# Optimization experiments

Hardware: AMD Instinct MI355X
Metric: run time of the kernel (lower is better)

The kernel has to match this reference:

```python
import jax, jax.numpy as jnp
import numpy as np


def setup_inputs() -> dict:
    key = jax.random.key(0)
    ks = jax.random.split(key, 6)
    B, H, W, C = 8, 128, 128, 256
    x = jax.random.normal(ks[0], (B, H, W), dtype=jnp.float32)
    atten_x_full = jax.random.normal(ks[1], (B, H, W, W), dtype=jnp.float32)
    atten_y_full = jax.random.normal(ks[2], (B, W, H, H), dtype=jnp.float32)
    value_full = jax.random.normal(ks[3], (B, H, W, C), dtype=jnp.float32)
    # nn.Parameter init: shift = |randn|, bias = -|randn|
    shift = jnp.abs(jax.random.normal(ks[4], (1,), dtype=jnp.float32))
    bias = -jnp.abs(jax.random.normal(ks[5], (1,), dtype=jnp.float32))
    return {"x": x, "atten_x_full": atten_x_full, "atten_y_full": atten_y_full,
            "value_full": value_full, "shift": shift, "bias": bias}


def reference(x, atten_x_full, atten_y_full, value_full, shift, bias):
    H, W = x.shape[1], x.shape[2]
    # Gaussian distance biases: gx[c, h] = -(shift*(h-c)^2 + bias), gy[r, w] likewise
    hw = jnp.arange(W, dtype=jnp.float32)
    hh = jnp.arange(H, dtype=jnp.float32)
    gx = -(shift[0] * (hw[None, :] - hw[:, None]) ** 2 + bias[0])  # [W, W]
    gy = -(shift[0] * (hh[None, :] - hh[:, None]) ** 2 + bias[0])  # [H, H]
    # atten_x_full indexed [b, r, c, k] -> add gx[c, k]; softmax over k (row direction)
    Ax = jax.nn.softmax(atten_x_full + gx[None, None, :, :], axis=-1)  # [B,H,W,W]
    # atten_y_full indexed [b, c, r, k] -> add gy[r, k]; softmax over k (col direction)
    Ay = jax.nn.softmax(atten_y_full + gy[None, None, :, :], axis=-1)  # [B,W,H,H]
    out = (jnp.einsum('brck,brkd->brcd', Ax, value_full)
           + jnp.einsum('bcrk,bkcd->brcd', Ay, value_full))  # [B,H,W,C]
    return out
```

## Files before the change

### kernel.cpp

```cpp
#include <hip/hip_runtime.h>
#include <hip/hip_bf16.h>

typedef __attribute__((ext_vector_type(8))) short short8;
typedef __attribute__((ext_vector_type(4))) float floatx4;
typedef __attribute__((ext_vector_type(2))) float floatx2;

#define LDK 136

__device__ __forceinline__ unsigned short f2bf(float x) {
    unsigned u = __builtin_bit_cast(unsigned, x);
    return (unsigned short)((u + 0x7fffu + ((u >> 16) & 1u)) >> 16);
}

template <bool ACCUM>
__global__ __launch_bounds__(512) void gtrans(
    const float* __restrict__ atten, const float* __restrict__ value,
    float* __restrict__ out, const float* __restrict__ shiftp,
    const float* __restrict__ biasp, int s0, int s1)
{
    __shared__ short Buf[128 * LDK];

    const int bi   = blockIdx.x;
    const int b    = bi >> 7;
    const int i    = bi & 127;
    const int tid  = threadIdx.x;
    const int lane = tid & 63;
    const int w    = tid >> 6;

    const float shift = shiftp[0];
    const float bias  = biasp[0];

    const float* abase = atten + (size_t)bi * (128 * 128);
    const float* vbase = value + (size_t)b * (128 * 128 * 256) + (size_t)i * s0;
    float*       obase = out   + (size_t)b * (128 * 128 * 256) + (size_t)i * s0;

    {
        floatx2 v[16];
#pragma unroll
        for (int j = 0; j < 16; ++j) {
            int c = w * 16 + j;
            v[j] = *(const floatx2*)(abase + c * 128 + 2 * lane);
        }
#pragma unroll
        for (int j = 0; j < 16; ++j) {
            int c = w * 16 + j;
            float d0 = (float)(2 * lane)     - (float)c;
            float d1 = (float)(2 * lane + 1) - (float)c;
            float a0 = v[j].x - (shift * d0 * d0 + bias);
            float a1 = v[j].y - (shift * d1 * d1 + bias);
            float m = fmaxf(a0, a1);
#pragma unroll
            for (int s = 1; s < 64; s <<= 1) m = fmaxf(m, __shfl_xor(m, s, 64));
            float e0 = __expf(a0 - m);
            float e1 = __expf(a1 - m);
            float ssum = e0 + e1;
#pragma unroll
            for (int s = 1; s < 64; s <<= 1) ssum += __shfl_xor(ssum, s, 64);
            float r = 1.0f / ssum;
            unsigned p = (unsigned)f2bf(e0 * r) | ((unsigned)f2bf(e1 * r) << 16);
            *(unsigned*)(&Buf[c * LDK + 2 * lane]) = p;
        }
    }
    __syncthreads();

    short8 bfrag[4];
    {
        int n  = w * 16 + (lane & 15);
        int kq = (lane >> 4) * 8;
#pragma unroll
        for (int ks = 0; ks < 4; ++ks)
            bfrag[ks] = *(const short8*)(&Buf[n * LDK + ks * 32 + kq]);
    }
    __syncthreads();

    floatx4 acc[8];
    const int am = lane & 15;
    const int kq = (lane >> 4) * 8;
#pragma unroll
    for (int half = 0; half < 2; ++half) {
        {
            floatx2 vv[16];
#pragma unroll
            for (int j = 0; j < 16; ++j) {
                int k = w * 16 + j;
                vv[j] = *(const floatx2*)(vbase + (size_t)k * s1 + half * 128 + 2 * lane);
            }
#pragma unroll
            for (int j = 0; j < 16; ++j) {
                int k  = w * 16 + j;
                int dl = 2 * lane;
                Buf[dl * LDK + k]       = (short)f2bf(vv[j].x);
                Buf[(dl + 1) * LDK + k] = (short)f2bf(vv[j].y);
            }
        }
        __syncthreads();

#pragma unroll
        for (int t = 0; t < 8; ++t) acc[t] = (floatx4)0.0f;

#pragma unroll
        for (int ks = 0; ks < 4; ++ks) {
#pragma unroll
            for (int t = 0; t < 8; ++t) {
                short8 af = *(const short8*)(&Buf[(t * 16 + am) * LDK + ks * 32 + kq]);
                acc[t] = __builtin_amdgcn_mfma_f32_16x16x32_bf16(af, bfrag[ks], acc[t], 0, 0, 0);
            }
        }

        {
            int n = w * 16 + (lane & 15);
            float* orow = obase + (size_t)n * s1 + half * 128 + (lane >> 4) * 4;
#pragma unroll
            for (int t = 0; t < 8; ++t) {
                float* p = orow + t * 16;
                floatx4 res = acc[t];
                if (ACCUM) {
                    floatx4 old = *(const floatx4*)p;
                    res = res + old;
                }
                *(floatx4*)p = res;
            }
        }
        __syncthreads();
    }
}

extern "C" void kernel_launch(void* const* d_in, const int* in_sizes, int n_in,
                              void* d_out, int out_size, void* d_ws, size_t ws_size,
                              hipStream_t stream) {
    const float* atten_x = (const float*)d_in[1];
    const float* atten_y = (const float*)d_in[2];
    const float* value   = (const float*)d_in[3];
    const float* shiftp  = (const float*)d_in[4];
    const float* biasp   = (const float*)d_in[5];
    float* out = (float*)d_out;

    dim3 grid(1024), block(512);
    gtrans<false><<<grid, block, 0, stream>>>(atten_x, value, out, shiftp, biasp,
                                              128 * 256, 256);
    gtrans<true><<<grid, block, 0, stream>>>(atten_y, value, out, shiftp, biasp,
                                             256, 128 * 256);
}
```

Measured before the change: 409.2 us.

## Compute softmax in MFMA fragment layout, prefetch value halves, swizzle LDS

The softmax is now computed directly in the MFMA B-fragment layout, using float4 loads and a 4-lane shuffle reduction, so the LDS round trip for the attention matrix is gone. Value tiles are loaded as float4 and written to LDS as packed short8 with an XOR swizzle, which removes the scalar transposed stores. The second half of the value tile is prefetched while the first half's MFMAs run. A minimum-blocks launch bound of 4 is added, which may push register use down or cause spills.

```diff
diff --git a/kernel.cpp b/kernel.cpp
--- a/kernel.cpp
+++ b/kernel.cpp
@@ -3,7 +3,6 @@
 
 typedef __attribute__((ext_vector_type(8))) short short8;
 typedef __attribute__((ext_vector_type(4))) float floatx4;
-typedef __attribute__((ext_vector_type(2))) float floatx2;
 
 #define LDK 136
 
@@ -13,7 +12,7 @@
 }
 
 template <bool ACCUM>
-__global__ __launch_bounds__(512) void gtrans(
+__global__ __launch_bounds__(512, 4) void gtrans(
     const float* __restrict__ atten, const float* __restrict__ value,
     float* __restrict__ out, const float* __restrict__ shiftp,
     const float* __restrict__ biasp, int s0, int s1)
@@ -34,94 +33,127 @@
     const float* vbase = value + (size_t)b * (128 * 128 * 256) + (size_t)i * s0;
     float*       obase = out   + (size_t)b * (128 * 128 * 256) + (size_t)i * s0;
 
+    const int nl  = w * 16 + (lane & 15);
+    const int kq  = (lane >> 4) * 8;
+    const int kvb = w * 16 + 8 * (lane >> 5);
+    const int dvb = 4 * (lane & 31);
+
+    floatx4 av[8];
     {
-        floatx2 v[16];
+        const float* arow = abase + nl * 128 + kq;
 #pragma unroll
-        for (int j = 0; j < 16; ++j) {
-            int c = w * 16 + j;
-            v[j] = *(const floatx2*)(abase + c * 128 + 2 * lane);
+        for (int ks = 0; ks < 4; ++ks) {
+            av[2 * ks]     = *(const floatx4*)(arow + ks * 32);
+            av[2 * ks + 1] = *(const floatx4*)(arow + ks * 32 + 4);
         }
+    }
+    floatx4 vv[8];
 #pragma unroll
-        for (int j = 0; j < 16; ++j) {
-            int c = w * 16 + j;
-            float d0 = (float)(2 * lane)     - (float)c;
-            float d1 = (float)(2 * lane + 1) - (float)c;
-            float a0 = v[j].x - (shift * d0 * d0 + bias);
-            float a1 = v[j].y - (shift * d1 * d1 + bias);
-            float m = fmaxf(a0, a1);
+    for (int t = 0; t < 8; ++t)
+        vv[t] = *(const floatx4*)(vbase + (size_t)(kvb + t) * s1 + dvb);
+
+    short8 bfrag[4];
+    {
+        float m = -1e30f;
 #pragma unroll
-            for (int s = 1; s < 64; s <<= 1) m = fmaxf(m, __shfl_xor(m, s, 64));
-            float e0 = __expf(a0 - m);
-            float e1 = __expf(a1 - m);
-            float ssum = e0 + e1;
+        for (int ks = 0; ks < 4; ++ks)
 #pragma unroll
-            for (int s = 1; s < 64; s <<= 1) ssum += __shfl_xor(ssum, s, 64);
-            float r = 1.0f / ssum;
-            unsigned p = (unsigned)f2bf(e0 * r) | ((unsigned)f2bf(e1 * r) << 16);
-            *(unsigned*)(&Buf[c * LDK + 2 * lane]) = p;
+            for (int h = 0; h < 2; ++h)
+#pragma unroll
+                for (int e = 0; e < 4; ++e) {
+                    float kf = (float)(ks * 32 + kq + h * 4 + e);
+                    float d  = kf - (float)nl;
+                    float v  = av[2 * ks + h][e] - (shift * d * d + bias);
+                    av[2 * ks + h][e] = v;
+                    m = fmaxf(m, v);
+                }
+        m = fmaxf(m, __shfl_xor(m, 16, 64));
+        m = fmaxf(m, __shfl_xor(m, 32, 64));
+        float s = 0.0f;
+#pragma unroll
+        for (int t = 0; t < 8; ++t)
+#pragma unroll
+            for (int e = 0; e < 4; ++e) {
+                float ex = __expf(av[t][e] - m);
+                av[t][e] = ex;
+                s += ex;
+            }
+        s += __shfl_xor(s, 16, 64);
+        s += __shfl_xor(s, 32, 64);
+        float r = 1.0f / s;
+#pragma unroll
+        for (int ks = 0; ks < 4; ++ks)
+#pragma unroll
+            for (int h = 0; h < 2; ++h)
+#pragma unroll
+                for (int e = 0; e < 4; ++e)
+                    bfrag[ks][h * 4 + e] = (short)f2bf(av[2 * ks + h][e] * r);
+    }
+
+    auto stageV = [&](const floatx4* vp) {
+#pragma unroll
+        for (int j = 0; j < 4; ++j) {
+            int row = dvb + j;
+            int cb  = (kvb >> 3) ^ ((row >> 2) & 15);
+            short8 p;
+#pragma unroll
+            for (int t = 0; t < 8; ++t) p[t] = (short)f2bf(vp[t][j]);
+            *(short8*)(&Buf[row * LDK + cb * 8]) = p;
+        }
+    };
+    stageV(vv);
+    __syncthreads();
+
+    floatx4 vu[8];
+#pragma unroll
+    for (int t = 0; t < 8; ++t)
+        vu[t] = *(const floatx4*)(vbase + (size_t)(kvb + t) * s1 + 128 + dvb);
+
+    const int am = lane & 15;
+    floatx4 acc[8];
+#pragma unroll
+    for (int t = 0; t < 8; ++t) acc[t] = (floatx4)0.0f;
+#pragma unroll
+    for (int ks = 0; ks < 4; ++ks) {
+#pragma unroll
+        for (int t = 0; t < 8; ++t) {
+            int row = t * 16 + am;
+            int cb  = (ks * 4 + (lane >> 4)) ^ ((row >> 2) & 15);
+            short8 af = *(const short8*)(&Buf[row * LDK + cb * 8]);
+            acc[t] = __builtin_amdgcn_mfma_f32_16x16x32_bf16(af, bfrag[ks], acc[t], 0, 0, 0);
         }
     }
     __syncthreads();
-
-    short8 bfrag[4];
-    {
-        int n  = w * 16 + (lane & 15);
-        int kq = (lane >> 4) * 8;
-#pragma unroll
-        for (int ks = 0; ks < 4; ++ks)
-            bfrag[ks] = *(const short8*)(&Buf[n * LDK + ks * 32 + kq]);
-    }
+    stageV(vu);
     __syncthreads();
 
-    floatx4 acc[8];
-    const int am = lane & 15;
-    const int kq = (lane >> 4) * 8;
+    float* orow = obase + (size_t)nl * s1 + (lane >> 4) * 4;
 #pragma unroll
-    for (int half = 0; half < 2; ++half) {
-        {
-            floatx2 vv[16];
-#pragma unroll
-            for (int j = 0; j < 16; ++j) {
-                int k = w * 16 + j;
-                vv[j] = *(const floatx2*)(vbase + (size_t)k * s1 + half * 128 + 2 * lane);
-            }
-#pragma unroll
-            for (int j = 0; j < 16; ++j) {
-                int k  = w * 16 + j;
-                int dl = 2 * lane;
-                Buf[dl * LDK + k]       = (short)f2bf(vv[j].x);
-                Buf[(dl + 1) * LDK + k] = (short)f2bf(vv[j].y);
-            }
-        }
-        __syncthreads();
+    for (int t = 0; t < 8; ++t) {
+        float* p = orow + t * 16;
+        floatx4 res = acc[t];
+        if (ACCUM) res = res + *(const floatx4*)p;
+        *(floatx4*)p = res;
+    }
 
 #pragma unroll
-        for (int t = 0; t < 8; ++t) acc[t] = (floatx4)0.0f;
-
+    for (int t = 0; t < 8; ++t) acc[t] = (floatx4)0.0f;
 #pragma unroll
-        for (int ks = 0; ks < 4; ++ks) {
+    for (int ks = 0; ks < 4; ++ks) {
 #pragma unroll
-            for (int t = 0; t < 8; ++t) {
-                short8 af = *(const short8*)(&Buf[(t * 16 + am) * LDK + ks * 32 + kq]);
-                acc[t] = __builtin_amdgcn_mfma_f32_16x16x32_bf16(af, bfrag[ks], acc[t], 0, 0, 0);
-            }
+        for (int t = 0; t < 8; ++t) {
+            int row = t * 16 + am;
+            int cb  = (ks * 4 + (lane >> 4)) ^ ((row >> 2) & 15);
+            short8 af = *(const short8*)(&Buf[row * LDK + cb * 8]);
+            acc[t] = __builtin_amdgcn_mfma_f32_16x16x32_bf16(af, bfrag[ks], acc[t], 0, 0, 0);
         }
-
-        {
-            int n = w * 16 + (lane & 15);
-            float* orow = obase + (size_t)n * s1 + half * 128 + (lane >> 4) * 4;
+    }
 #pragma unroll
-            for (int t = 0; t < 8; ++t) {
-                float* p = orow + t * 16;
-                floatx4 res = acc[t];
-                if (ACCUM) {
-                    floatx4 old = *(const floatx4*)p;
-                    res = res + old;
-                }
-                *(floatx4*)p = res;
-            }
-        }
-        __syncthreads();
+    for (int t = 0; t < 8; ++t) {
+        float* p = orow + 128 + t * 16;
+        floatx4 res = acc[t];
+        if (ACCUM) res = res + *(const floatx4*)p;
+        *(floatx4*)p = res;
     }
 }
 
```

Result: slower. 430.2 us (+5.1%).
